# Optimization experiments

Measured on AMD Instinct MI355X. Metric: run time of the kernel, lower is better.

## Reference

```python
import jax, jax.numpy as jnp
import numpy as np

B, L, NC, D = 4, 2048, 4096, 128
ITERS = 4
NHEAD = 8
T = L // 2
C2 = 2 * D


def _ln(x, g, b, eps=1e-5):
    m = jnp.mean(x, axis=-1, keepdims=True)
    v = jnp.var(x, axis=-1, keepdims=True)
    return (x - m) * jax.lax.rsqrt(v + eps) * g + b


def _mlp3(x, W1, b1, W2, b2, W3, b3):
    h = jax.nn.relu(x @ W1 + b1)
    h = jax.nn.relu(h @ W2 + b2)
    return h @ W3 + b3


def _lstm(inp, h, c, Wih, Whh, gi, bi, gh, bh, gc, bc):
    gates = _ln(inp @ Wih, gi, bi) + _ln(h @ Whh, gh, bh)
    i, f, g, o = jnp.split(gates, 4, axis=-1)
    cy = _ln(jax.nn.sigmoid(f) * c + jax.nn.sigmoid(i) * jnp.tanh(g), gc, bc)
    hy = jax.nn.sigmoid(o) * jnp.tanh(cy)
    return hy, cy


def _flip(x):
    # flip matrix with full literal counts == permutation swapping pos/neg halves
    half = x.shape[1] // 2
    return jnp.concatenate([x[:, half:], x[:, :half]], axis=1)


def setup_inputs():
    key = jax.random.key(0)
    ks = iter(jax.random.split(key, 64))
    def xav(fi, fo):
        s = float(np.sqrt(6.0 / (fi + fo)))
        return jax.random.uniform(next(ks), (fi, fo), jnp.float32, -s, s)
    def rn(*shape):
        return jax.random.normal(next(ks), shape, jnp.float32)
    inp = {}
    inp['adjacency_matrices'] = (jax.random.uniform(next(ks), (B, L, NC)) < 0.03).astype(jnp.float32)
    inp['batch_lit_counts'] = jnp.full((B,), L, dtype=jnp.int32)
    inp['L_init'] = rn(1, D) / np.sqrt(D).astype(np.float32)
    inp['C_init'] = rn(1, D) / np.sqrt(D).astype(np.float32)
    for p in ('LC', 'CL'):
        for i in (1, 2, 3):
            inp[p + '_W' + str(i)] = xav(D, D)
            inp[p + '_b' + str(i)] = jnp.full((D,), 0.01, jnp.float32)
    for p, isz in (('Lu', 2 * D), ('Cu', D)):
        inp[p + '_Wih'] = rn(isz, 4 * D)  # torch uses raw randn for LSTM weights
        inp[p + '_Whh'] = rn(D, 4 * D)
        for ln, n in (('lni', 4 * D), ('lnh', 4 * D), ('lnc', D)):
            inp[p + '_' + ln + '_g'] = jnp.ones((n,), jnp.float32)
            inp[p + '_' + ln + '_b'] = jnp.zeros((n,), jnp.float32)
    for p in ('k', 'q', 'v'):
        inp['att_W' + p] = xav(C2, C2)
        inp['att_b' + p] = jnp.zeros((C2,), jnp.float32)
    for p in ('asn', 'vote'):
        inp[p + '_W1'] = xav(C2, D)
        inp[p + '_b1'] = jnp.full((D,), 0.01, jnp.float32)
        inp[p + '_W2'] = xav(D, 1)
        inp[p + '_b2'] = jnp.full((1,), 0.01, jnp.float32)
    return inp


def reference(adjacency_matrices, batch_lit_counts, L_init, C_init,
              LC_W1, LC_b1, LC_W2, LC_b2, LC_W3, LC_b3,
              CL_W1, CL_b1, CL_W2, CL_b2, CL_W3, CL_b3,
              Lu_Wih, Lu_Whh, Lu_lni_g, Lu_lni_b, Lu_lnh_g, Lu_lnh_b, Lu_lnc_g, Lu_lnc_b,
              Cu_Wih, Cu_Whh, Cu_lni_g, Cu_lni_b, Cu_lnh_g, Cu_lnh_b, Cu_lnc_g, Cu_lnc_b,
              att_Wk, att_bk, att_Wq, att_bq, att_Wv, att_bv,
              asn_W1, asn_b1, asn_W2, asn_b2, vote_W1, vote_b1, vote_W2, vote_b2):
    A = adjacency_matrices
    Bb, Ll, Cc = A.shape
    Lh = jnp.broadcast_to(L_init, (Bb, Ll, D))
    Lc = jnp.zeros_like(Lh)
    Ch = jnp.broadcast_to(C_init, (Bb, Cc, D))
    Cxc = jnp.zeros_like(Ch)
    for _ in range(ITERS):
        # literal -> clause messages (gather via A^T)
        LC = jnp.einsum('blc,bld->bcd', A, _mlp3(Lh, LC_W1, LC_b1, LC_W2, LC_b2, LC_W3, LC_b3))
        Ch, Cxc = _lstm(LC, Ch, Cxc, Cu_Wih, Cu_Whh, Cu_lni_g, Cu_lni_b, Cu_lnh_g, Cu_lnh_b, Cu_lnc_g, Cu_lnc_b)
        # clause -> literal messages (scatter via A)
        CL = jnp.einsum('blc,bcd->bld', A, _mlp3(Ch, CL_W1, CL_b1, CL_W2, CL_b2, CL_W3, CL_b3))
        Lh, Lc = _lstm(jnp.concatenate([CL, _flip(Lh)], axis=-1), Lh, Lc,
                       Lu_Wih, Lu_Whh, Lu_lni_g, Lu_lni_b, Lu_lnh_g, Lu_lnh_b, Lu_lnc_g, Lu_lnc_b)
    # readout [h_l ; h_{~l}], positive literals only
    read = jnp.concatenate([Lh, _flip(Lh)], axis=-1)[:, :T]  # [B,T,2D]
    half = batch_lit_counts // 2
    mask = (jnp.arange(T)[None, :] < half[:, None]).astype(read.dtype)  # [B,T]
    read = read * mask[:, :, None]
    hd = C2 // NHEAD
    def heads(x, W, b):
        return (x @ W + b).reshape(Bb, T, NHEAD, hd).transpose(0, 2, 1, 3)
    k = heads(read, att_Wk, att_bk)
    q = heads(read, att_Wq, att_bq)
    v = heads(read, att_Wv, att_bv)
    att = jnp.einsum('bhtd,bhsd->bhts', q, k) * (1.0 / np.sqrt(hd))
    sq = (mask[:, None, :, None] * mask[:, None, None, :]) > 0  # [B,1,T,T]
    att = jnp.where(sq, att, -jnp.inf)
    att = jax.nn.softmax(att, axis=-1)
    att = jnp.where(jnp.isnan(att), 0.0, att)
    y = jnp.einsum('bhts,bhsd->bhtd', att, v).transpose(0, 2, 1, 3).reshape(Bb, T, C2)
    def head_mlp(x, W1, b1, W2, b2):
        return jax.nn.sigmoid(jax.nn.relu(x @ W1 + b1) @ W2 + b2)[..., 0]
    assignments = head_mlp(y, asn_W1, asn_b1, asn_W2, asn_b2) * mask  # [B,T]
    vote_vals = head_mlp(y, vote_W1, vote_b1, vote_W2, vote_b2)
    votes = jnp.sum(vote_vals * mask, axis=1) / jnp.maximum(jnp.sum(mask, axis=1), 1.0)
    return votes, assignments
```

## Files before the change

kernel.cpp:

```cpp
#include <hip/hip_runtime.h>


#define B_    4
#define L_    2048
#define NC_   4096
#define D_    128
#define ITERS_ 4
#define NH_   8
#define T_    1024
#define C2_   256
#define HD_   32
#define BL_   (B_*L_)
#define BNC_  (B_*NC_)

typedef unsigned short u16;
typedef __attribute__((ext_vector_type(8))) short b16x8;
typedef __attribute__((ext_vector_type(4))) float f32x4;

#define MFMA_BF16(a,b,c) __builtin_amdgcn_mfma_f32_16x16x32_bf16((a),(b),(c),0,0,0)

static __device__ __forceinline__ float bf2f(u16 u){
  union{unsigned int i; float f;} x; x.i = ((unsigned int)u) << 16; return x.f;
}
static __device__ __forceinline__ u16 f2bf(float f){
// ... 45 lines not shown
               ksb[NPJ_], dh[NPJ_], dl[NPJ_]; };

__global__ __launch_bounds__(256) void k_prep(PJobs pj, u16* __restrict__ up,
                                              const int* __restrict__ flag){
  int jj = blockIdx.y;
  unsigned n = pj.n[jj];
  unsigned g = blockIdx.x*256 + threadIdx.x;
  if (g >= n) return;
  unsigned j = g & 7, lane = (g>>3)&63;
  unsigned ksb = pj.ksb[jj];
  unsigned ks = (g>>9) & ((1u<<ksb)-1u);
  unsigned nt = g >> (9+ksb);
  unsigned ncol = nt*16 + (lane&15);
  unsigned k = pj.koff[jj] + ks*32 + ((lane>>4)&3)*8 + j;
  unsigned si = k*pj.N[jj] + ncol;
  float v;
  if (*flag) v = bf2f(((const u16*)pj.src[jj])[si]);
  else       v = ((const float*)pj.src[jj])[si];
  u16 h,l; split2(v, h, l);
  up[pj.dh[jj] + g] = h;
  up[pj.dl[jj] + g] = l;
}

__global__ __launch_bounds__(256) void k_init(float* __restrict__ h, float* __restrict__ c,
                                              const float* __restrict__ init, int n){
  int i = blockIdx.x*256 + threadIdx.x;
  if (i < n){ h[i] = init[i & (D_-1)]; c[i] = 0.f; }
}

__global__ void k_zero_u(unsigned* __restrict__ p, int n){
  int i = blockIdx.x*256 + threadIdx.x; if (i < n) p[i] = 0u;
}
__global__ void k_zero(float* p, int n){
  int i = blockIdx.x*64 + threadIdx.x; if (i < n) p[i] = 0.f;
}

__global__ __launch_bounds__(128) void k_pack(const void* __restrict__ A,
    unsigned* __restrict__ bits, unsigned* __restrict__ cnt_l,
    const int* __restrict__ flag){
  const int row = blockIdx.x, w = threadIdx.x;
  unsigned m = 0;
  if (*flag){
    const ushort4* p = (const ushort4*)A + (size_t)row*(NC_/4) + w*8;
    #pragma unroll
    for (int i = 0; i < 8; i++){
      ushort4 u = p[i];
      m |= (unsigned)(u.x != 0) << (i*4);
      m |= (unsigned)(u.y != 0) << (i*4+1);
      m |= (unsigned)(u.z != 0) << (i*4+2);
      m |= (unsigned)(u.w != 0) << (i*4+3);
// ... 62 lines not shown
    int j = __ffs(m) - 1; m &= m - 1;
    val_l[base++] = (u16)(w*32 + j);
    atomicAdd(cnt_c + cb + j, 1u);
  }
}

__global__ __launch_bounds__(256) void k_fill_c(const unsigned* __restrict__ bits,
    const unsigned* __restrict__ off_c, unsigned* __restrict__ cur_c,
    u16* __restrict__ val_c){
  int g = blockIdx.x*256 + threadIdx.x;
  unsigned m = bits[g];
  int row = g >> 7, w = g & 127;
  int b = row >> 11, l = row & (L_-1);
  unsigned cb = ((unsigned)b << 12) + w*32;
  while (m){
    int j = __ffs(m) - 1; m &= m - 1;
    unsigned idx = cb + j;
    unsigned pos = atomicAdd(cur_c + idx, 1u);
    val_c[off_c[idx] + pos] = (u16)l;
  }
}

__global__ __launch_bounds__(256) void k_spmm(const unsigned* __restrict__ off,
    const u16* __restrict__ val, const float* __restrict__ M, float* __restrict__ out,
    int sh1, int sh2){
  int row  = blockIdx.x*4 + (threadIdx.x >> 6);
  int lane = threadIdx.x & 63;
  unsigned p0 = off[row], p1 = off[row+1];
  const float2* Mp = (const float2*)M + (((size_t)(row >> sh1) << sh2) * 64) + lane;
  float x = 0.f, y = 0.f;
  for (unsigned p = p0; p < p1; ++p){
    float2 v = Mp[(size_t)val[p] * 64];
    x += v.x; y += v.y;
  }
  float2 r; r.x = x; r.y = y;
  ((float2*)out)[(size_t)row*64 + lane] = r;
}

__global__ __launch_bounds__(512) void k_mlp3m(const float* __restrict__ X,
    const u16* __restrict__ W1h, const u16* __restrict__ W1l,
    const u16* __restrict__ W2h, const u16* __restrict__ W2l,
    const u16* __restrict__ W3h, const u16* __restrict__ W3l,
    const float* __restrict__ b1, const float* __restrict__ b2,
    const float* __restrict__ b3, float* __restrict__ Y)
{
  __shared__ __align__(16) u16 Ah[32*136];
  __shared__ __align__(16) u16 Al[32*136];
  const int tid = threadIdx.x, lane = tid & 63, wv = tid >> 6;
  const int quad = lane >> 4, l15 = lane & 15;
  const int r0 = blockIdx.x * 32;
  {
    int row = tid >> 4, c0 = (tid & 15)*8;
    const float4* src = (const float4*)(X + (size_t)(r0+row)*128 + c0);
    float4 v0 = src[0], v1 = src[1];
    u16 h,l;
    split2(v0.x,h,l); Ah[row*136+c0]  =h; Al[row*136+c0]  =l;
    split2(v0.y,h,l); Ah[row*136+c0+1]=h; Al[row*136+c0+1]=l;
    split2(v0.z,h,l); Ah[row*136+c0+2]=h; Al[row*136+c0+2]=l;
    split2(v0.w,h,l); Ah[row*136+c0+3]=h; Al[row*136+c0+3]=l;
    split2(v1.x,h,l); Ah[row*136+c0+4]=h; Al[row*136+c0+4]=l;
    split2(v1.y,h,l); Ah[row*136+c0+5]=h; Al[row*136+c0+5]=l;
    split2(v1.z,h,l); Ah[row*136+c0+6]=h; Al[row*136+c0+6]=l;
    split2(v1.w,h,l); Ah[row*136+c0+7]=h; Al[row*136+c0+7]=l;
  }
  __syncthreads();
  const u16* Whs[3] = {W1h, W2h, W3h};
  const u16* Wls[3] = {W1l, W2l, W3l};
  const float* bs[3] = {b1, b2, b3};
  #pragma unroll
  for (int layer = 0; layer < 3; layer++){
    f32x4 acc[2] = {};
    #pragma unroll
    for (int ks = 0; ks < 4; ks++){
      b16x8 a_h[2], a_l[2];
      #pragma unroll
      for (int mt = 0; mt < 2; mt++){
        int ao = (mt*16 + l15)*136 + ks*32 + quad*8;
        a_h[mt] = *(const b16x8*)(Ah + ao);
        a_l[mt] = *(const b16x8*)(Al + ao);
      }
      size_t bo = (size_t)((wv*4 + ks)*64 + lane)*8;
      b16x8 bh = *(const b16x8*)(Whs[layer] + bo);
      b16x8 bl = *(const b16x8*)(Wls[layer] + bo);
      #pragma unroll
      for (int mt = 0; mt < 2; mt++){
        acc[mt] = MFMA_BF16(a_h[mt], bh, acc[mt]);
        acc[mt] = MFMA_BF16(a_h[mt], bl, acc[mt]);
        acc[mt] = MFMA_BF16(a_l[mt], bh, acc[mt]);
      }
    }
    int col = wv*16 + l15;
    if (layer < 2){
      float bb = bs[layer][col];
      __syncthreads();
      #pragma unroll
      for (int mt = 0; mt < 2; mt++)
        #pragma unroll
        for (int r = 0; r < 4; r++){
          int row = mt*16 + quad*4 + r;
          float v = fmaxf(acc[mt][r] + bb, 0.f);
          u16 h,l; split2(v,h,l);
          Ah[row*136 + col] = h; Al[row*136 + col] = l;
        }
      __syncthreads();
    } else {
      float bb = bs[2][col];
      #pragma unroll
      for (int mt = 0; mt < 2; mt++)
        #pragma unroll
        for (int r = 0; r < 4; r++){
          int row = mt*16 + quad*4 + r;
          Y[(size_t)(r0+row)*128 + col] = acc[mt][r] + bb;
        }
    }
  }
}

template<int NSEG>
__global__ __launch_bounds__(512) void k_lstm_mfma(
    const float* __restrict__ A0, const float* __restrict__ A1, const float* __restrict__ A2,
    int flip1,
    const u16* __restrict__ W0h, const u16* __restrict__ W0l,
    const u16* __restrict__ W1h, const u16* __restrict__ W1l,
    const u16* __restrict__ W2h, const u16* __restrict__ W2l,
    const float* __restrict__ lni_g, const float* __restrict__ lni_b,
    const float* __restrict__ lnh_g, const float* __restrict__ lnh_b,
    const float* __restrict__ lnc_g, const float* __restrict__ lnc_b,
    const float* __restrict__ c_in, float* __restrict__ c_out,
    float* __restrict__ h_out)
{
  __shared__ __align__(16) float G[32*516];
  __shared__ float red[8][32][4];
  __shared__ float st[32][4];
  u16* Ah = (u16*)G;
  u16* Al = Ah + 32*136;
  const int tid = threadIdx.x, lane = tid & 63, wv = tid >> 6;
  const int quad = lane >> 4, l15 = lane & 15;
  const int r0 = blockIdx.x * 32;

  f32x4 acc1[2][4] = {}, acc2[2][4] = {};

  #pragma unroll
  for (int s = 0; s < NSEG; ++s){
    const float* Ap = (s==0) ? A0 : ((s==1) ? A1 : A2);
    const u16* Wh = (s==0) ? W0h : ((s==1) ? W1h : W2h);
    const u16* Wl = (s==0) ? W0l : ((s==1) ? W1l : W2l);
    const int fm = (s==1) ? flip1 : 0;
    __syncthreads();
    {
      int row = tid >> 4, c0 = (tid & 15)*8;
      int arow = (r0 + row) ^ fm;
      const float4* src = (const float4*)(Ap + (size_t)arow*128 + c0);
      float4 v0 = src[0], v1 = src[1];
      u16 h,l;
      split2(v0.x,h,l); Ah[row*136+c0]  =h; Al[row*136+c0]  =l;
      split2(v0.y,h,l); Ah[row*136+c0+1]=h; Al[row*136+c0+1]=l;
      split2(v0.z,h,l); Ah[row*136+c0+2]=h; Al[row*136+c0+2]=l;
      split2(v0.w,h,l); Ah[row*136+c0+3]=h; Al[row*136+c0+3]=l;
      split2(v1.x,h,l); Ah[row*136+c0+4]=h; Al[row*136+c0+4]=l;
      split2(v1.y,h,l); Ah[row*136+c0+5]=h; Al[row*136+c0+5]=l;
      split2(v1.z,h,l); Ah[row*136+c0+6]=h; Al[row*136+c0+6]=l;
      split2(v1.w,h,l); Ah[row*136+c0+7]=h; Al[row*136+c0+7]=l;
    }
    __syncthreads();
    f32x4 (*accp)[4] = (s == NSEG-1) ? acc2 : acc1;
    #pragma unroll
    for (int ks = 0; ks < 4; ks++){
      b16x8 a_h[2], a_l[2];
      #pragma unroll
      for (int mt = 0; mt < 2; mt++){
        int ao = (mt*16 + l15)*136 + ks*32 + quad*8;
        a_h[mt] = *(const b16x8*)(Ah + ao);
        a_l[mt] = *(const b16x8*)(Al + ao);
      }
      #pragma unroll
      for (int ntl = 0; ntl < 4; ntl++){
        int nt = wv*4 + ntl;
        size_t bo = (size_t)((nt*4 + ks)*64 + lane)*8;
        b16x8 bh = *(const b16x8*)(Wh + bo);
        b16x8 bl = *(const b16x8*)(Wl + bo);
        #pragma unroll
        for (int mt = 0; mt < 2; mt++){
          accp[mt][ntl] = MFMA_BF16(a_h[mt], bh, accp[mt][ntl]);
          accp[mt][ntl] = MFMA_BF16(a_h[mt], bl, accp[mt][ntl]);
          accp[mt][ntl] = MFMA_BF16(a_l[mt], bh, accp[mt][ntl]);
        }
      }
    }
  }

  #pragma unroll
  for (int mt = 0; mt < 2; mt++)
    #pragma unroll
    for (int r = 0; r < 4; r++){
      float s1=0.f, q1=0.f, s2=0.f, q2=0.f;
      #pragma unroll
// ... 51 lines not shown
  #pragma unroll
  for (int i = 0; i < 4; i++){
    int row = wv*4 + i;
    int rg = r0 + row;
    float cp[2], sc = 0.f, qc = 0.f;
    #pragma unroll
    for (int jj = 0; jj < 2; jj++){
      int c = lane + 64*jj;
      float iv = sigm(G[row*516 + c]);
      float fv = sigm(G[row*516 + 128 + c]);
      float gv = tanhf(G[row*516 + 256 + c]);
      cp[jj] = fv * c_in[(size_t)rg*128 + c] + iv*gv;
      sc += cp[jj]; qc += cp[jj]*cp[jj];
    }
    #pragma unroll
    for (int m = 1; m < 64; m <<= 1){ sc += __shfl_xor(sc, m); qc += __shfl_xor(qc, m); }
    float mc = sc*i128, vc = fmaxf(qc*i128 - mc*mc, 0.f), rsc = rsqrtf(vc + 1e-5f);
    #pragma unroll
    for (int jj = 0; jj < 2; jj++){
      int c = lane + 64*jj;
      float cy = (cp[jj]-mc)*rsc*(jj ? lcg1 : lcg0) + (jj ? lcb1 : lcb0);
      c_out[(size_t)rg*128 + c] = cy;
      float ov = sigm(G[row*516 + 384 + c]);
      h_out[(size_t)rg*128 + c] = ov*tanhf(cy);
    }
  }
}

template<int NT, int NSPLIT, int KK32, int ACT, int GATHER>
__global__ __launch_bounds__(512) void k_gemm_mfma(const float* __restrict__ A,
    const u16* __restrict__ Wh, const u16* __restrict__ Wl,
    const float* __restrict__ bias, float* __restrict__ Y,
    const int* __restrict__ counts)
{
  const int NTOT = NSPLIT*8*NT*16;
  const int LDA = KK32*32 + 8;
  __shared__ __align__(16) u16 Ah[32*(KK32*32+8)];
  __shared__ __align__(16) u16 Al[32*(KK32*32+8)];
  const int tid = threadIdx.x, lane = tid & 63, wv = tid >> 6;
  const int quad = lane >> 4, l15 = lane & 15;
  const int r0 = blockIdx.x * 32, by = blockIdx.y;
  {
    int row = tid >> 4, c0 = (tid & 15)*(KK32*2);
    if (GATHER){
      int r = r0 + row; int b = r >> 10; int t = r & 1023;
      int half = counts[b] / 2; if (half > T_) half = T_;
      float msk = (t < half) ? 1.f : 0.f;
      #pragma unroll
      for (int q4 = 0; q4 < KK32/2; q4++){
        int c = c0 + q4*4;
        const float* src = A + ((size_t)(b*L_ + t + ((c >= 128) ? T_ : 0))*128 + (c & 127));
        float4 v = *(const float4*)src;
        u16 h,l;
        split2(v.x*msk,h,l); Ah[row*LDA+c]  =h; Al[row*LDA+c]  =l;
        split2(v.y*msk,h,l); Ah[row*LDA+c+1]=h; Al[row*LDA+c+1]=l;
        split2(v.z*msk,h,l); Ah[row*LDA+c+2]=h; Al[row*LDA+c+2]=l;
        split2(v.w*msk,h,l); Ah[row*LDA+c+3]=h; Al[row*LDA+c+3]=l;
      }
    } else {
      const float4* src = (const float4*)(A + (size_t)(r0+row)*(KK32*32) + c0);
      #pragma unroll
      for (int q4 = 0; q4 < KK32/2; q4++){
        float4 v = src[q4]; int c = c0 + q4*4;
        u16 h,l;
        split2(v.x,h,l); Ah[row*LDA+c]  =h; Al[row*LDA+c]  =l;
        split2(v.y,h,l); Ah[row*LDA+c+1]=h; Al[row*LDA+c+1]=l;
        split2(v.z,h,l); Ah[row*LDA+c+2]=h; Al[row*LDA+c+2]=l;
        split2(v.w,h,l); Ah[row*LDA+c+3]=h; Al[row*LDA+c+3]=l;
      }
    }
  }
  __syncthreads();
  f32x4 acc[2][NT] = {};
  #pragma unroll
  for (int ks = 0; ks < KK32; ks++){
    b16x8 a_h[2], a_l[2];
    #pragma unroll
    for (int mt = 0; mt < 2; mt++){
      int ao = (mt*16 + l15)*LDA + ks*32 + quad*8;
      a_h[mt] = *(const b16x8*)(Ah + ao);
      a_l[mt] = *(const b16x8*)(Al + ao);
    }
    #pragma unroll
    for (int ntl = 0; ntl < NT; ntl++){
      int nt = by*(8*NT) + wv*NT + ntl;
      size_t bo = (size_t)((nt*KK32 + ks)*64 + lane)*8;
      b16x8 bh = *(const b16x8*)(Wh + bo);
      b16x8 bl = *(const b16x8*)(Wl + bo);
      #pragma unroll
      for (int mt = 0; mt < 2; mt++){
        acc[mt][ntl] = MFMA_BF16(a_h[mt], bh, acc[mt][ntl]);
        acc[mt][ntl] = MFMA_BF16(a_h[mt], bl, acc[mt][ntl]);
        acc[mt][ntl] = MFMA_BF16(a_l[mt], bh, acc[mt][ntl]);
      }
    }
  }
  #pragma unroll
  for (int mt = 0; mt < 2; mt++)
    #pragma unroll
    for (int ntl = 0; ntl < NT; ntl++){
      int colg = by*(8*NT*16) + wv*(NT*16) + ntl*16 + l15;
      float bb = bias[colg];
      #pragma unroll
      for (int r = 0; r < 4; r++){
        int row = mt*16 + quad*4 + r;
        float v = acc[mt][ntl][r] + bb;
        if (ACT) v = fmaxf(v, 0.f);
        Y[(size_t)(r0+row)*NTOT + colg] = v;
      }
    }
}

__global__ __launch_bounds__(512) void k_qkv_gemm(const float* __restrict__ A,
    const u16* __restrict__ Wh, const u16* __restrict__ Wl,
    const float* __restrict__ bias,
    u16* __restrict__ Qh, u16* __restrict__ Ql,
    u16* __restrict__ Kh, u16* __restrict__ Kl,
    u16* __restrict__ Vth, u16* __restrict__ Vtl,
    const int* __restrict__ counts)
{
  const int KK32 = 8, NT = 3;
  const int LDA = KK32*32 + 8;
  __shared__ __align__(16) u16 Ah[32*(KK32*32+8)];
  __shared__ __align__(16) u16 Al[32*(KK32*32+8)];
  const int tid = threadIdx.x, lane = tid & 63, wv = tid >> 6;
  const int quad = lane >> 4, l15 = lane & 15;
  const int r0 = blockIdx.x * 32, by = blockIdx.y;
  {
    int row = tid >> 4, c0 = (tid & 15)*(KK32*2);
    int r = r0 + row; int b = r >> 10; int t = r & 1023;
    int half = counts[b] / 2; if (half > T_) half = T_;
    float msk = (t < half) ? 1.f : 0.f;
    #pragma unroll
    for (int q4 = 0; q4 < KK32/2; q4++){
      int c = c0 + q4*4;
      const float* src = A + ((size_t)(b*L_ + t + ((c >= 128) ? T_ : 0))*128 + (c & 127));
      float4 v = *(const float4*)src;
      u16 h,l;
      split2(v.x*msk,h,l); Ah[row*LDA+c]  =h; Al[row*LDA+c]  =l;
      split2(v.y*msk,h,l); Ah[row*LDA+c+1]=h; Al[row*LDA+c+1]=l;
      split2(v.z*msk,h,l); Ah[row*LDA+c+2]=h; Al[row*LDA+c+2]=l;
      split2(v.w*msk,h,l); Ah[row*LDA+c+3]=h; Al[row*LDA+c+3]=l;
    }
  }
  __syncthreads();
  f32x4 acc[2][NT] = {};
  #pragma unroll
  for (int ks = 0; ks < KK32; ks++){
    b16x8 a_h[2], a_l[2];
    #pragma unroll
    for (int mt = 0; mt < 2; mt++){
      int ao = (mt*16 + l15)*LDA + ks*32 + quad*8;
      a_h[mt] = *(const b16x8*)(Ah + ao);
      a_l[mt] = *(const b16x8*)(Al + ao);
    }
    #pragma unroll
    for (int ntl = 0; ntl < NT; ntl++){
      int nt = by*(8*NT) + wv*NT + ntl;
      size_t bo = (size_t)((nt*KK32 + ks)*64 + lane)*8;
      b16x8 bh = *(const b16x8*)(Wh + bo);
      b16x8 bl = *(const b16x8*)(Wl + bo);
      #pragma unroll
      for (int mt = 0; mt < 2; mt++){
        acc[mt][ntl] = MFMA_BF16(a_h[mt], bh, acc[mt][ntl]);
        acc[mt][ntl] = MFMA_BF16(a_h[mt], bl, acc[mt][ntl]);
        acc[mt][ntl] = MFMA_BF16(a_l[mt], bh, acc[mt][ntl]);
      }
    }
  }
  #pragma unroll
  for (int mt = 0; mt < 2; mt++)
    #pragma unroll
    for (int ntl = 0; ntl < NT; ntl++){
      int colg = by*(8*NT*16) + wv*(NT*16) + ntl*16 + l15;
      float bb = bias[colg];
      #pragma unroll
      for (int r = 0; r < 4; r++){
        int row = r0 + mt*16 + quad*4 + r;
        int bI = row >> 10, t = row & 1023;
        float v = acc[mt][ntl][r] + bb;
        u16 hh, ll; split2(v, hh, ll);
        if (colg < 256){
          int h8 = colg >> 5, k = colg & 31;
          size_t idx = ((size_t)(bI*NH_ + h8)*1024 + t)*32 + k;
          Qh[idx] = hh; Ql[idx] = ll;
        } else if (colg < 512){
          int c = colg - 256; int h8 = c >> 5, k = c & 31;
          size_t idx = ((size_t)(bI*NH_ + h8)*1024 + t)*32 + k;
          Kh[idx] = hh; Kl[idx] = ll;
        } else {
          int c = colg - 512; int h8 = c >> 5, n = c & 31;
          size_t idx = ((size_t)(bI*NH_ + h8)*32 + n)*1024 + t;
          Vth[idx] = hh; Vtl[idx] = ll;
        }
      }
    }
}

__global__ __launch_bounds__(256) void k_attn_mfma(
    const u16* __restrict__ Qh, const u16* __restrict__ Ql,
    const u16* __restrict__ Kh, const u16* __restrict__ Kl,
    const u16* __restrict__ Vth, const u16* __restrict__ Vtl,
    const int* __restrict__ counts, float* __restrict__ y)
{
  const int b = blockIdx.z, h = blockIdx.y, t0 = blockIdx.x*64;
  int half = counts[b] / 2; if (half > T_) half = T_; if (half < 0) half = 0;
  const int tid = threadIdx.x, lane = tid & 63, w = tid >> 6;
  const int quad = lane >> 4, l15 = lane & 15;
  __shared__ __align__(16) u16 Pb[4][2][16*72];
  const int tw = t0 + w*16;
  const size_t bh = (size_t)(b*NH_ + h)*32768;
  const u16* qhb = Qh + bh; const u16* qlb = Ql + bh;
  const u16* khb = Kh + bh; const u16* klb = Kl + bh;
  const u16* vhb = Vth + bh; const u16* vlb = Vtl + bh;

  b16x8 qah = *(const b16x8*)(qhb + (size_t)(tw + l15)*32 + quad*8);
  b16x8 qal = *(const b16x8*)(qlb + (size_t)(tw + l15)*32 + quad*8);

  f32x4 accO[2] = {};
  float mst[4], lst[4];
  #pragma unroll
  for (int r = 0; r < 4; r++){ mst[r] = -3e38f; lst[r] = 0.f; }
  const float scale = 0.17677669529663687f;
  const int ntile = (t0 < half) ? ((half + 63) >> 6) : 0;

  for (int st = 0; st < ntile; ++st){
// ... 46 lines not shown
      accO[1][r] *= alpha[r];
    }
    #pragma unroll
    for (int kc = 0; kc < 2; kc++){
      b16x8 ph = *(const b16x8*)&Pb[w][0][l15*72 + kc*32 + quad*8];
      b16x8 pl = *(const b16x8*)&Pb[w][1][l15*72 + kc*32 + quad*8];
      #pragma unroll
      for (int nt = 0; nt < 2; nt++){
        const size_t vo = (size_t)(nt*16 + l15)*1024 + s0 + kc*32 + quad*8;
        b16x8 vh8 = *(const b16x8*)(vhb + vo);
        b16x8 vl8 = *(const b16x8*)(vlb + vo);
        accO[nt] = MFMA_BF16(ph, vh8, accO[nt]);
        accO[nt] = MFMA_BF16(ph, vl8, accO[nt]);
        accO[nt] = MFMA_BF16(pl, vh8, accO[nt]);
      }
    }
  }

  #pragma unroll
  for (int r = 0; r < 4; r++){
    int t = tw + quad*4 + r;
    float inv = (t < half && lst[r] > 0.f) ? 1.f/lst[r] : 0.f;
    #pragma unroll
    for (int nt = 0; nt < 2; nt++)
      y[(size_t)(b*T_ + t)*C2_ + h*HD_ + nt*16 + l15] = accO[nt][r]*inv;
  }
}

__global__ __launch_bounds__(128) void k_final(const float* __restrict__ hv,
    const float* __restrict__ aW2, const float* __restrict__ ab2,
    const float* __restrict__ vW2, const float* __restrict__ vb2,
    const int* __restrict__ counts, void* __restrict__ outv,
    float* __restrict__ vote_sum, const int* __restrict__ flag)
{
  int row = blockIdx.x, tid = threadIdx.x;
  int b = row / T_, t = row - b*T_;
  int half = counts[b] / 2; if (half > T_) half = T_;
  float pa = hv[(size_t)row*256 + tid]       * aW2[tid];
  float pv = hv[(size_t)row*256 + 128 + tid] * vW2[tid];
  #pragma unroll
  for (int off = 32; off > 0; off >>= 1){ pa += __shfl_down(pa, off); pv += __shfl_down(pv, off); }
  __shared__ float r[2][2];
  int wid = tid >> 6, lane = tid & 63;
  if (lane == 0){ r[0][wid] = pa; r[1][wid] = pv; }
  __syncthreads();
  if (tid == 0){
    float a  = sigm(r[0][0] + r[0][1] + ab2[0]);
    float vv = sigm(r[1][0] + r[1][1] + vb2[0]);
    bool mk = (t < half);
// ... 25 lines not shown

  const size_t M1 = (size_t)1048576;
  const size_t NEED = (5*M1 + M1 + 2*M1 + 2*M1 + 700416 + 16416 + 8224
                       + 16384 + 8192 + 520000 + 520000 + 32) * sizeof(float);
  if (ws_size < NEED) return;

  float* ws = (float*)d_ws;
  float* R    = ws;
  float* Lc   = R + 5*M1;
  float* Ch   = Lc + M1;
  float* Cc   = Ch + 2*M1;
  float* wp   = Cc + 2*M1;
  unsigned* off_c = (unsigned*)(wp + 700416);
  unsigned* off_l = off_c + 16416;
  unsigned* cnt_c = off_l + 8224;
  unsigned* cnt_l = cnt_c + 16384;
  u16* val_c = (u16*)(cnt_l + 8192);
  u16* val_l = (u16*)((float*)val_c + 520000);
  float* tail = (float*)val_l + 520000;
  float* vote_sum = tail;
  int* flag = (int*)(tail + 8);
  unsigned* bits = (unsigned*)R;

  float* R0 = R, *R1 = R + M1, *R2 = R + 2*M1, *R3 = R + 3*M1, *R4 = R + 4*M1;

  k_detect<<<1, 256, 0, stream>>>((const unsigned int*)A_adj, flag);

  CJobs cj;
  int ncj = 0;
  unsigned off = 0;
  auto cadd = [&](int idx, unsigned n)->float*{
    cj.src[ncj] = d_in[idx]; cj.n[ncj] = n; cj.off[ncj] = off;
    float* p = wp + off; off += (n + 3u) & ~3u; ncj++; return p;
  };
  float* Linit = cadd(2, 128);
  float* Cinit = cadd(3, 128);
  float *LC_b1 = cadd(5, 128), *LC_b2 = cadd(7, 128), *LC_b3 = cadd(9, 128);
  float *CL_b1 = cadd(11,128), *CL_b2 = cadd(13,128), *CL_b3 = cadd(15,128);
  float *Lu_lni_g = cadd(18,512), *Lu_lni_b = cadd(19,512);
  float *Lu_lnh_g = cadd(20,512), *Lu_lnh_b = cadd(21,512);
  float *Lu_lnc_g = cadd(22,128), *Lu_lnc_b = cadd(23,128);
  float *Cu_lni_g = cadd(26,512), *Cu_lni_b = cadd(27,512);
  float *Cu_lnh_g = cadd(28,512), *Cu_lnh_b = cadd(29,512);
  float *Cu_lnc_g = cadd(30,128), *Cu_lnc_b = cadd(31,128);
  float *asn_W2 = cadd(40,128), *asn_b2 = cadd(41,1);
  float *vote_W2 = cadd(44,128), *vote_b2 = cadd(45,1);
  float* bqkv = wp + off;
// ... 32 lines not shown
  solo(16,65536,512,0,  2,&lwa_h,&lwa_l);
  solo(16,65536,512,128,2,&lwb_h,&lwb_l);
  solo(17,65536,512,0,2,&lwhh_h,&lwhh_l);
  const u16* wqkv_h = up + uoff;
  const u16* wqkv_l = up + uoff + 196608;
  padd(34, 65536, 256, 0, 3, uoff,           uoff+196608);
  padd(32, 65536, 256, 0, 3, uoff+65536,     uoff+196608+65536);
  padd(36, 65536, 256, 0, 3, uoff+131072,    uoff+196608+131072);
  uoff += 393216;
  const u16* whv_h = up + uoff;
  const u16* whv_l = up + uoff + 65536;
  padd(38, 32768, 128, 0, 3, uoff,        uoff+65536);
  padd(42, 32768, 128, 0, 3, uoff+32768,  uoff+65536+32768);
  uoff += 131072;
  { dim3 g(256, NPJ_); k_prep<<<g, 256, 0, stream>>>(pj, up, flag); }

  k_zero_u<<<(16384+255)/256, 256, 0, stream>>>(cnt_c, 16384);
  k_pack<<<BL_, 128, 0, stream>>>(A_adj, bits, cnt_l, flag);
  k_scan<<<1, 256, 0, stream>>>(cnt_l, off_l, 8192);
  k_fill_l<<<BL_, 128, 0, stream>>>(bits, off_l, val_l, cnt_c);
  k_scan<<<1, 256, 0, stream>>>(cnt_c, off_c, 16384);
  k_fill_c<<<4096, 256, 0, stream>>>(bits, off_c, cnt_c, val_c);

  k_init<<<(BL_*D_)/256, 256, 0, stream>>>(R0, Lc, Linit, BL_*D_);
  k_init<<<(BNC_*D_)/256, 256, 0, stream>>>(Ch, Cc, Cinit, BNC_*D_);

  for (int it = 0; it < ITERS_; ++it){
    bool ev = ((it & 1) == 0);
    float* cur  = ev ? R0 : R4;
    float* msgL = ev ? R1 : R0;
    float* LCb  = ev ? R2 : R1;
    float* msgC = LCb;
    float* CLb  = ev ? R1 : R3;
    float* nxt  = ev ? R4 : R0;

    k_mlp3m<<<BL_/32, 512, 0, stream>>>(cur, lc1h,lc1l, lc2h,lc2l, lc3h,lc3l,
                                        LC_b1, LC_b2, LC_b3, msgL);
    k_spmm<<<BNC_/4, 256, 0, stream>>>(off_c, val_c, msgL, LCb, 12, 11);
    k_lstm_mfma<2><<<BNC_/32, 512, 0, stream>>>(LCb, Ch, nullptr, 0,
        cwih_h, cwih_l, cwhh_h, cwhh_l, nullptr, nullptr,
        Cu_lni_g, Cu_lni_b, Cu_lnh_g, Cu_lnh_b, Cu_lnc_g, Cu_lnc_b, Cc, Cc, Ch);
    k_mlp3m<<<BNC_/32, 512, 0, stream>>>(Ch, cl1h,cl1l, cl2h,cl2l, cl3h,cl3l,
                                         CL_b1, CL_b2, CL_b3, msgC);
    k_spmm<<<BL_/4, 256, 0, stream>>>(off_l, val_l, msgC, CLb, 11, 12);
    k_lstm_mfma<3><<<BL_/32, 512, 0, stream>>>(CLb, cur, cur, 1024,
        lwa_h, lwa_l, lwb_h, lwb_l, lwhh_h, lwhh_l,
        Lu_lni_g, Lu_lni_b, Lu_lnh_g, Lu_lnh_b, Lu_lnc_g, Lu_lnc_b, Lc, Lc, nxt);
  }
  float* Lh = R0;

  u16* qk = (u16*)Ch;
  u16* Qh_ = qk;           u16* Ql_ = qk + 1048576;
  u16* Kh_ = qk + 2097152; u16* Kl_ = qk + 3145728;
  u16* vt = (u16*)Cc;
  u16* Vth_ = vt;          u16* Vtl_ = vt + 1048576;
  float* yb = R1;
  float* hv = R2;

  { dim3 g((B_*T_)/32, 2);
    k_qkv_gemm<<<g, 512, 0, stream>>>(Lh, wqkv_h, wqkv_l, bqkv,
                                      Qh_, Ql_, Kh_, Kl_, Vth_, Vtl_, counts); }
  { dim3 g(T_/64, NH_, B_);
    k_attn_mfma<<<g, 256, 0, stream>>>(Qh_, Ql_, Kh_, Kl_, Vth_, Vtl_, counts, yb); }
  { dim3 g((B_*T_)/32, 2);
    k_gemm_mfma<1,2,8,1,0><<<g, 512, 0, stream>>>(yb, whv_h, whv_l, bhv, hv, counts); }
  k_zero<<<1, 64, 0, stream>>>(vote_sum, B_);
  k_final<<<B_*T_, 128, 0, stream>>>(hv, asn_W2, asn_b2, vote_W2, vote_b2,
                                     counts, d_out, vote_sum, flag);
  k_votes<<<1, 64, 0, stream>>>(vote_sum, counts, d_out, flag);
}
```

Before: 1.593 ms.

## Store activations pre-split as bf16 hi/lo pairs to skip LDS staging

```diff
diff --git a/kernel.cpp b/kernel.cpp
--- a/kernel.cpp
+++ b/kernel.cpp
@@ -91,10 +91,13 @@
   up[pj.dl[jj] + g] = l;
 }
 
-__global__ __launch_bounds__(256) void k_init(float* __restrict__ h, float* __restrict__ c,
-                                              const float* __restrict__ init, int n){
+__global__ __launch_bounds__(256) void k_init_h(u16* __restrict__ hh, u16* __restrict__ hl,
+    float* __restrict__ c, const float* __restrict__ init, int n){
   int i = blockIdx.x*256 + threadIdx.x;
-  if (i < n){ h[i] = init[i & (D_-1)]; c[i] = 0.f; }
+  if (i < n){
+    u16 h,l; split2(init[i & (D_-1)], h, l);
+    hh[i] = h; hl[i] = l; c[i] = 0.f;
+  }
 }
 
 __global__ void k_zero_u(unsigned* __restrict__ p, int n){
@@ -203,8 +206,8 @@
 }
 
 __global__ __launch_bounds__(256) void k_spmm(const unsigned* __restrict__ off,
-    const u16* __restrict__ val, const float* __restrict__ M, float* __restrict__ out,
-    int sh1, int sh2){
+    const u16* __restrict__ val, const float* __restrict__ M,
+    u16* __restrict__ outh, u16* __restrict__ outl, int sh1, int sh2){
   int row  = blockIdx.x*4 + (threadIdx.x >> 6);
   int lane = threadIdx.x & 63;
   unsigned p0 = off[row], p1 = off[row+1];
@@ -214,11 +217,13 @@
     float2 v = Mp[(size_t)val[p] * 64];
     x += v.x; y += v.y;
   }
-  float2 r; r.x = x; r.y = y;
-  ((float2*)out)[(size_t)row*64 + lane] = r;
-}
-
-__global__ __launch_bounds__(512) void k_mlp3m(const float* __restrict__ X,
+  u16 hx,lx,hy,ly; split2(x,hx,lx); split2(y,hy,ly);
+  ((unsigned*)outh)[(size_t)row*64 + lane] = (unsigned)hx | ((unsigned)hy << 16);
+  ((unsigned*)outl)[(size_t)row*64 + lane] = (unsigned)lx | ((unsigned)ly << 16);
+}
+
+__global__ __launch_bounds__(512) void k_mlp3m(const u16* __restrict__ Xh,
+    const u16* __restrict__ Xl,
     const u16* __restrict__ W1h, const u16* __restrict__ W1l,
     const u16* __restrict__ W2h, const u16* __restrict__ W2l,
     const u16* __restrict__ W3h, const u16* __restrict__ W3l,
@@ -230,21 +235,6 @@
   const int tid = threadIdx.x, lane = tid & 63, wv = tid >> 6;
   const int quad = lane >> 4, l15 = lane & 15;
   const int r0 = blockIdx.x * 32;
-  {
-    int row = tid >> 4, c0 = (tid & 15)*8;
-    const float4* src = (const float4*)(X + (size_t)(r0+row)*128 + c0);
-    float4 v0 = src[0], v1 = src[1];
-    u16 h,l;
-    split2(v0.x,h,l); Ah[row*136+c0]  =h; Al[row*136+c0]  =l;
-    split2(v0.y,h,l); Ah[row*136+c0+1]=h; Al[row*136+c0+1]=l;
-    split2(v0.z,h,l); Ah[row*136+c0+2]=h; Al[row*136+c0+2]=l;
-    split2(v0.w,h,l); Ah[row*136+c0+3]=h; Al[row*136+c0+3]=l;
-    split2(v1.x,h,l); Ah[row*136+c0+4]=h; Al[row*136+c0+4]=l;
-    split2(v1.y,h,l); Ah[row*136+c0+5]=h; Al[row*136+c0+5]=l;
-    split2(v1.z,h,l); Ah[row*136+c0+6]=h; Al[row*136+c0+6]=l;
-    split2(v1.w,h,l); Ah[row*136+c0+7]=h; Al[row*136+c0+7]=l;
-  }
-  __syncthreads();
   const u16* Whs[3] = {W1h, W2h, W3h};
   const u16* Wls[3] = {W1l, W2l, W3l};
   const float* bs[3] = {b1, b2, b3};
@@ -256,9 +246,15 @@
       b16x8 a_h[2], a_l[2];
       #pragma unroll
       for (int mt = 0; mt < 2; mt++){
-        int ao = (mt*16 + l15)*136 + ks*32 + quad*8;
-        a_h[mt] = *(const b16x8*)(Ah + ao);
-        a_l[mt] = *(const b16x8*)(Al + ao);
+        if (layer == 0){
+          size_t ao = (size_t)(r0 + mt*16 + l15)*128 + ks*32 + quad*8;
+          a_h[mt] = *(const b16x8*)(Xh + ao);
+          a_l[mt] = *(const b16x8*)(Xl + ao);
+        } else {
+          int ao = (mt*16 + l15)*136 + ks*32 + quad*8;
+          a_h[mt] = *(const b16x8*)(Ah + ao);
+          a_l[mt] = *(const b16x8*)(Al + ao);
+        }
       }
       size_t bo = (size_t)((wv*4 + ks)*64 + lane)*8;
       b16x8 bh = *(const b16x8*)(Whs[layer] + bo);
@@ -299,7 +295,9 @@
 
 template<int NSEG>
 __global__ __launch_bounds__(512) void k_lstm_mfma(
-    const float* __restrict__ A0, const float* __restrict__ A1, const float* __restrict__ A2,
+    const u16* __restrict__ A0h, const u16* __restrict__ A0l,
+    const u16* __restrict__ A1h, const u16* __restrict__ A1l,
+    const u16* __restrict__ A2h, const u16* __restrict__ A2l,
     int flip1,
     const u16* __restrict__ W0h, const u16* __restrict__ W0l,
     const u16* __restrict__ W1h, const u16* __restrict__ W1l,
@@ -308,13 +306,11 @@
     const float* __restrict__ lnh_g, const float* __restrict__ lnh_b,
     const float* __restrict__ lnc_g, const float* __restrict__ lnc_b,
     const float* __restrict__ c_in, float* __restrict__ c_out,
-    float* __restrict__ h_out)
+    u16* __restrict__ h_outh, u16* __restrict__ h_outl)
 {
   __shared__ __align__(16) float G[32*516];
   __shared__ float red[8][32][4];
   __shared__ float st[32][4];
-  u16* Ah = (u16*)G;
-  u16* Al = Ah + 32*136;
   const int tid = threadIdx.x, lane = tid & 63, wv = tid >> 6;
   const int quad = lane >> 4, l15 = lane & 15;
   const int r0 = blockIdx.x * 32;
@@ -323,36 +319,20 @@
 
   #pragma unroll
   for (int s = 0; s < NSEG; ++s){
-    const float* Ap = (s==0) ? A0 : ((s==1) ? A1 : A2);
-    const u16* Wh = (s==0) ? W0h : ((s==1) ? W1h : W2h);
-    const u16* Wl = (s==0) ? W0l : ((s==1) ? W1l : W2l);
+    const u16* Aph = (s==0) ? A0h : ((s==1) ? A1h : A2h);
+    const u16* Apl = (s==0) ? A0l : ((s==1) ? A1l : A2l);
+    const u16* Wh  = (s==0) ? W0h : ((s==1) ? W1h : W2h);
+    const u16* Wl  = (s==0) ? W0l : ((s==1) ? W1l : W2l);
     const int fm = (s==1) ? flip1 : 0;
-    __syncthreads();
-    {
-      int row = tid >> 4, c0 = (tid & 15)*8;
-      int arow = (r0 + row) ^ fm;
-      const float4* src = (const float4*)(Ap + (size_t)arow*128 + c0);
-      float4 v0 = src[0], v1 = src[1];
-      u16 h,l;
-      split2(v0.x,h,l); Ah[row*136+c0]  =h; Al[row*136+c0]  =l;
-      split2(v0.y,h,l); Ah[row*136+c0+1]=h; Al[row*136+c0+1]=l;
-      split2(v0.z,h,l); Ah[row*136+c0+2]=h; Al[row*136+c0+2]=l;
-      split2(v0.w,h,l); Ah[row*136+c0+3]=h; Al[row*136+c0+3]=l;
-      split2(v1.x,h,l); Ah[row*136+c0+4]=h; Al[row*136+c0+4]=l;
-      split2(v1.y,h,l); Ah[row*136+c0+5]=h; Al[row*136+c0+5]=l;
-      split2(v1.z,h,l); Ah[row*136+c0+6]=h; Al[row*136+c0+6]=l;
-      split2(v1.w,h,l); Ah[row*136+c0+7]=h; Al[row*136+c0+7]=l;
-    }
-    __syncthreads();
     f32x4 (*accp)[4] = (s == NSEG-1) ? acc2 : acc1;
     #pragma unroll
     for (int ks = 0; ks < 4; ks++){
       b16x8 a_h[2], a_l[2];
       #pragma unroll
       for (int mt = 0; mt < 2; mt++){
-        int ao = (mt*16 + l15)*136 + ks*32 + quad*8;
-        a_h[mt] = *(const b16x8*)(Ah + ao);
-        a_l[mt] = *(const b16x8*)(Al + ao);
+        size_t ao = (size_t)((r0 + mt*16 + l15) ^ fm)*128 + ks*32 + quad*8;
+        a_h[mt] = *(const b16x8*)(Aph + ao);
+        a_l[mt] = *(const b16x8*)(Apl + ao);
       }
       #pragma unroll
       for (int ntl = 0; ntl < 4; ntl++){
@@ -450,96 +430,16 @@
       float cy = (cp[jj]-mc)*rsc*(jj ? lcg1 : lcg0) + (jj ? lcb1 : lcb0);
       c_out[(size_t)rg*128 + c] = cy;
       float ov = sigm(G[row*516 + 384 + c]);
-      h_out[(size_t)rg*128 + c] = ov*tanhf(cy);
-    }
-  }
-}
-
-template<int NT, int NSPLIT, int KK32, int ACT, int GATHER>
-__global__ __launch_bounds__(512) void k_gemm_mfma(const float* __restrict__ A,
-    const u16* __restrict__ Wh, const u16* __restrict__ Wl,
-    const float* __restrict__ bias, float* __restrict__ Y,
-    const int* __restrict__ counts)
-{
-  const int NTOT = NSPLIT*8*NT*16;
-  const int LDA = KK32*32 + 8;
-  __shared__ __align__(16) u16 Ah[32*(KK32*32+8)];
-  __shared__ __align__(16) u16 Al[32*(KK32*32+8)];
-  const int tid = threadIdx.x, lane = tid & 63, wv = tid >> 6;
-  const int quad = lane >> 4, l15 = lane & 15;
-  const int r0 = blockIdx.x * 32, by = blockIdx.y;
-  {
-    int row = tid >> 4, c0 = (tid & 15)*(KK32*2);
-    if (GATHER){
-      int r = r0 + row; int b = r >> 10; int t = r & 1023;
-      int half = counts[b] / 2; if (half > T_) half = T_;
-      float msk = (t < half) ? 1.f : 0.f;
-      #pragma unroll
-      for (int q4 = 0; q4 < KK32/2; q4++){
-        int c = c0 + q4*4;
-        const float* src = A + ((size_t)(b*L_ + t + ((c >= 128) ? T_ : 0))*128 + (c & 127));
-        float4 v = *(const float4*)src;
-        u16 h,l;
-        split2(v.x*msk,h,l); Ah[row*LDA+c]  =h; Al[row*LDA+c]  =l;
-        split2(v.y*msk,h,l); Ah[row*LDA+c+1]=h; Al[row*LDA+c+1]=l;
-        split2(v.z*msk,h,l); Ah[row*LDA+c+2]=h; Al[row*LDA+c+2]=l;
-        split2(v.w*msk,h,l); Ah[row*LDA+c+3]=h; Al[row*LDA+c+3]=l;
-      }
-    } else {
-      const float4* src = (const float4*)(A + (size_t)(r0+row)*(KK32*32) + c0);
-      #pragma unroll
-      for (int q4 = 0; q4 < KK32/2; q4++){
-        float4 v = src[q4]; int c = c0 + q4*4;
-        u16 h,l;
-        split2(v.x,h,l); Ah[row*LDA+c]  =h; Al[row*LDA+c]  =l;
-        split2(v.y,h,l); Ah[row*LDA+c+1]=h; Al[row*LDA+c+1]=l;
-        split2(v.z,h,l); Ah[row*LDA+c+2]=h; Al[row*LDA+c+2]=l;
-        split2(v.w,h,l); Ah[row*LDA+c+3]=h; Al[row*LDA+c+3]=l;
-      }
-    }
-  }
-  __syncthreads();
-  f32x4 acc[2][NT] = {};
-  #pragma unroll
-  for (int ks = 0; ks < KK32; ks++){
-    b16x8 a_h[2], a_l[2];
-    #pragma unroll
-    for (int mt = 0; mt < 2; mt++){
-      int ao = (mt*16 + l15)*LDA + ks*32 + quad*8;
-      a_h[mt] = *(const b16x8*)(Ah + ao);
-      a_l[mt] = *(const b16x8*)(Al + ao);
-    }
-    #pragma unroll
-    for (int ntl = 0; ntl < NT; ntl++){
-      int nt = by*(8*NT) + wv*NT + ntl;
-      size_t bo = (size_t)((nt*KK32 + ks)*64 + lane)*8;
-      b16x8 bh = *(const b16x8*)(Wh + bo);
-      b16x8 bl = *(const b16x8*)(Wl + bo);
-      #pragma unroll
-      for (int mt = 0; mt < 2; mt++){
-        acc[mt][ntl] = MFMA_BF16(a_h[mt], bh, acc[mt][ntl]);
-        acc[mt][ntl] = MFMA_BF16(a_h[mt], bl, acc[mt][ntl]);
-        acc[mt][ntl] = MFMA_BF16(a_l[mt], bh, acc[mt][ntl]);
-      }
-    }
-  }
-  #pragma unroll
-  for (int mt = 0; mt < 2; mt++)
-    #pragma unroll
-    for (int ntl = 0; ntl < NT; ntl++){
-      int colg = by*(8*NT*16) + wv*(NT*16) + ntl*16 + l15;
-      float bb = bias[colg];
-      #pragma unroll
-      for (int r = 0; r < 4; r++){
-        int row = mt*16 + quad*4 + r;
-        float v = acc[mt][ntl][r] + bb;
-        if (ACT) v = fmaxf(v, 0.f);
-        Y[(size_t)(r0+row)*NTOT + colg] = v;
-      }
-    }
-}
-
-__global__ __launch_bounds__(512) void k_qkv_gemm(const float* __restrict__ A,
+      float hval = ov*tanhf(cy);
+      u16 hh, ll; split2(hval, hh, ll);
+      h_outh[(size_t)rg*128 + c] = hh;
+      h_outl[(size_t)rg*128 + c] = ll;
+    }
+  }
+}
+
+__global__ __launch_bounds__(512) void k_qkv_gemm(const u16* __restrict__ Lhh,
+    const u16* __restrict__ Lhl,
     const u16* __restrict__ Wh, const u16* __restrict__ Wl,
     const float* __restrict__ bias,
     u16* __restrict__ Qh, u16* __restrict__ Ql,
@@ -547,45 +447,37 @@
     u16* __restrict__ Vth, u16* __restrict__ Vtl,
     const int* __restrict__ counts)
 {
-  const int KK32 = 8, NT = 3;
-  const int LDA = KK32*32 + 8;
-  __shared__ __align__(16) u16 Ah[32*(KK32*32+8)];
-  __shared__ __align__(16) u16 Al[32*(KK32*32+8)];
+  const int NT = 3;
   const int tid = threadIdx.x, lane = tid & 63, wv = tid >> 6;
   const int quad = lane >> 4, l15 = lane & 15;
   const int r0 = blockIdx.x * 32, by = blockIdx.y;
-  {
-    int row = tid >> 4, c0 = (tid & 15)*(KK32*2);
-    int r = r0 + row; int b = r >> 10; int t = r & 1023;
+  size_t off0[2], off1[2];
+  bool mk[2];
+  #pragma unroll
+  for (int mt = 0; mt < 2; mt++){
+    int r = r0 + mt*16 + l15;
+    int b = r >> 10, t = r & 1023;
     int half = counts[b] / 2; if (half > T_) half = T_;
-    float msk = (t < half) ? 1.f : 0.f;
-    #pragma unroll
-    for (int q4 = 0; q4 < KK32/2; q4++){
-      int c = c0 + q4*4;
-      const float* src = A + ((size_t)(b*L_ + t + ((c >= 128) ? T_ : 0))*128 + (c & 127));
-      float4 v = *(const float4*)src;
-      u16 h,l;
-      split2(v.x*msk,h,l); Ah[row*LDA+c]  =h; Al[row*LDA+c]  =l;
-      split2(v.y*msk,h,l); Ah[row*LDA+c+1]=h; Al[row*LDA+c+1]=l;
-      split2(v.z*msk,h,l); Ah[row*LDA+c+2]=h; Al[row*LDA+c+2]=l;
-      split2(v.w*msk,h,l); Ah[row*LDA+c+3]=h; Al[row*LDA+c+3]=l;
-    }
-  }
-  __syncthreads();
+    mk[mt] = (t < half);
+    off0[mt] = (size_t)(b*L_ + t)*128;
+    off1[mt] = (size_t)(b*L_ + t + T_)*128;
+  }
+  const b16x8 z = {};
   f32x4 acc[2][NT] = {};
   #pragma unroll
-  for (int ks = 0; ks < KK32; ks++){
+  for (int ks = 0; ks < 8; ks++){
+    const int kk = (ks & 3)*32 + quad*8;
     b16x8 a_h[2], a_l[2];
     #pragma unroll
     for (int mt = 0; mt < 2; mt++){
-      int ao = (mt*16 + l15)*LDA + ks*32 + quad*8;
-      a_h[mt] = *(const b16x8*)(Ah + ao);
-      a_l[mt] = *(const b16x8*)(Al + ao);
+      size_t ao = ((ks < 4) ? off0[mt] : off1[mt]) + kk;
+      a_h[mt] = mk[mt] ? *(const b16x8*)(Lhh + ao) : z;
+      a_l[mt] = mk[mt] ? *(const b16x8*)(Lhl + ao) : z;
     }
     #pragma unroll
     for (int ntl = 0; ntl < NT; ntl++){
       int nt = by*(8*NT) + wv*NT + ntl;
-      size_t bo = (size_t)((nt*KK32 + ks)*64 + lane)*8;
+      size_t bo = (size_t)((nt*8 + ks)*64 + lane)*8;
       b16x8 bh = *(const b16x8*)(Wh + bo);
       b16x8 bl = *(const b16x8*)(Wl + bo);
       #pragma unroll
@@ -629,7 +521,8 @@
     const u16* __restrict__ Qh, const u16* __restrict__ Ql,
     const u16* __restrict__ Kh, const u16* __restrict__ Kl,
     const u16* __restrict__ Vth, const u16* __restrict__ Vtl,
-    const int* __restrict__ counts, float* __restrict__ y)
+    const int* __restrict__ counts,
+    u16* __restrict__ yh, u16* __restrict__ yl)
 {
   const int b = blockIdx.z, h = blockIdx.y, t0 = blockIdx.x*64;
   int half = counts[b] / 2; if (half > T_) half = T_; if (half < 0) half = 0;
@@ -722,9 +615,52 @@
     int t = tw + quad*4 + r;
     float inv = (t < half && lst[r] > 0.f) ? 1.f/lst[r] : 0.f;
     #pragma unroll
-    for (int nt = 0; nt < 2; nt++)
-      y[(size_t)(b*T_ + t)*C2_ + h*HD_ + nt*16 + l15] = accO[nt][r]*inv;
-  }
+    for (int nt = 0; nt < 2; nt++){
+      u16 hh, ll; split2(accO[nt][r]*inv, hh, ll);
+      size_t yi = (size_t)(b*T_ + t)*C2_ + h*HD_ + nt*16 + l15;
+      yh[yi] = hh; yl[yi] = ll;
+    }
+  }
+}
+
+__global__ __launch_bounds__(512) void k_hv_gemm(const u16* __restrict__ yh,
+    const u16* __restrict__ yl,
+    const u16* __restrict__ Wh, const u16* __restrict__ Wl,
+    const float* __restrict__ bias, float* __restrict__ Y)
+{
+  const int tid = threadIdx.x, lane = tid & 63, wv = tid >> 6;
+  const int quad = lane >> 4, l15 = lane & 15;
+  const int r0 = blockIdx.x * 32, by = blockIdx.y;
+  f32x4 acc[2] = {};
+  #pragma unroll
+  for (int ks = 0; ks < 8; ks++){
+    b16x8 a_h[2], a_l[2];
+    #pragma unroll
+    for (int mt = 0; mt < 2; mt++){
+      size_t ao = (size_t)(r0 + mt*16 + l15)*256 + ks*32 + quad*8;
+      a_h[mt] = *(const b16x8*)(yh + ao);
+      a_l[mt] = *(const b16x8*)(yl + ao);
+    }
+    int nt = by*8 + wv;
+    size_t bo = (size_t)((nt*8 + ks)*64 + lane)*8;
+    b16x8 bh = *(const b16x8*)(Wh + bo);
+    b16x8 bl = *(const b16x8*)(Wl + bo);
+    #pragma unroll
+    for (int mt = 0; mt < 2; mt++){
+      acc[mt] = MFMA_BF16(a_h[mt], bh, acc[mt]);
+      acc[mt] = MFMA_BF16(a_h[mt], bl, acc[mt]);
+      acc[mt] = MFMA_BF16(a_l[mt], bh, acc[mt]);
+    }
+  }
+  int colg = by*128 + wv*16 + l15;
+  float bb = bias[colg];
+  #pragma unroll
+  for (int mt = 0; mt < 2; mt++)
+    #pragma unroll
+    for (int r = 0; r < 4; r++){
+      int row = mt*16 + quad*4 + r;
+      Y[(size_t)(r0+row)*256 + colg] = fmaxf(acc[mt][r] + bb, 0.f);
+    }
 }
 
 __global__ __launch_bounds__(128) void k_final(const float* __restrict__ hv,
@@ -796,7 +732,11 @@
   int* flag = (int*)(tail + 8);
   unsigned* bits = (unsigned*)R;
 
-  float* R0 = R, *R1 = R + M1, *R2 = R + 2*M1, *R3 = R + 3*M1, *R4 = R + 4*M1;
+  auto SH = [&](int i)->u16*{ return (u16*)(R + i*M1); };
+  auto SL = [&](int i)->u16*{ return (u16*)(R + i*M1) + M1; };
+
+  u16* Chh = (u16*)Ch; u16* Chl = Chh + 2*M1;
+  float* R0 = R, *R1 = R + M1, *R2 = R + 2*M1;
 
   k_detect<<<1, 256, 0, stream>>>((const unsigned int*)A_adj, flag);
 
@@ -875,48 +815,49 @@
   k_scan<<<1, 256, 0, stream>>>(cnt_c, off_c, 16384);
   k_fill_c<<<4096, 256, 0, stream>>>(bits, off_c, cnt_c, val_c);
 
-  k_init<<<(BL_*D_)/256, 256, 0, stream>>>(R0, Lc, Linit, BL_*D_);
-  k_init<<<(BNC_*D_)/256, 256, 0, stream>>>(Ch, Cc, Cinit, BNC_*D_);
+  k_init_h<<<(BL_*D_)/256, 256, 0, stream>>>(SH(0), SL(0), Lc, Linit, BL_*D_);
+  k_init_h<<<(BNC_*D_)/256, 256, 0, stream>>>(Chh, Chl, Cc, Cinit, BNC_*D_);
 
   for (int it = 0; it < ITERS_; ++it){
     bool ev = ((it & 1) == 0);
-    float* cur  = ev ? R0 : R4;
+    u16 *curh = ev ? SH(0) : SH(4), *curl = ev ? SL(0) : SL(4);
     float* msgL = ev ? R1 : R0;
-    float* LCb  = ev ? R2 : R1;
-    float* msgC = LCb;
-    float* CLb  = ev ? R1 : R3;
-    float* nxt  = ev ? R4 : R0;
-
-    k_mlp3m<<<BL_/32, 512, 0, stream>>>(cur, lc1h,lc1l, lc2h,lc2l, lc3h,lc3l,
+    u16 *LCbh = ev ? (u16*)(R+2*M1) : (u16*)(R+1*M1);
+    u16 *LCbl = ev ? (u16*)(R+3*M1) : (u16*)(R+2*M1);
+    float* msgC = ev ? (R+2*M1) : (R+1*M1);
+    u16 *CLbh = ev ? SH(1) : SH(3), *CLbl = ev ? SL(1) : SL(3);
+    u16 *nxth = ev ? SH(4) : SH(0), *nxtl = ev ? SL(4) : SL(0);
+
+    k_mlp3m<<<BL_/32, 512, 0, stream>>>(curh, curl, lc1h,lc1l, lc2h,lc2l, lc3h,lc3l,
                                         LC_b1, LC_b2, LC_b3, msgL);
-    k_spmm<<<BNC_/4, 256, 0, stream>>>(off_c, val_c, msgL, LCb, 12, 11);
-    k_lstm_mfma<2><<<BNC_/32, 512, 0, stream>>>(LCb, Ch, nullptr, 0,
+    k_spmm<<<BNC_/4, 256, 0, stream>>>(off_c, val_c, msgL, LCbh, LCbl, 12, 11);
+    k_lstm_mfma<2><<<BNC_/32, 512, 0, stream>>>(LCbh, LCbl, Chh, Chl, nullptr, nullptr, 0,
         cwih_h, cwih_l, cwhh_h, cwhh_l, nullptr, nullptr,
-        Cu_lni_g, Cu_lni_b, Cu_lnh_g, Cu_lnh_b, Cu_lnc_g, Cu_lnc_b, Cc, Cc, Ch);
-    k_mlp3m<<<BNC_/32, 512, 0, stream>>>(Ch, cl1h,cl1l, cl2h,cl2l, cl3h,cl3l,
+        Cu_lni_g, Cu_lni_b, Cu_lnh_g, Cu_lnh_b, Cu_lnc_g, Cu_lnc_b, Cc, Cc, Chh, Chl);
+    k_mlp3m<<<BNC_/32, 512, 0, stream>>>(Chh, Chl, cl1h,cl1l, cl2h,cl2l, cl3h,cl3l,
                                          CL_b1, CL_b2, CL_b3, msgC);
-    k_spmm<<<BL_/4, 256, 0, stream>>>(off_l, val_l, msgC, CLb, 11, 12);
-    k_lstm_mfma<3><<<BL_/32, 512, 0, stream>>>(CLb, cur, cur, 1024,
+    k_spmm<<<BL_/4, 256, 0, stream>>>(off_l, val_l, msgC, CLbh, CLbl, 11, 12);
+    k_lstm_mfma<3><<<BL_/32, 512, 0, stream>>>(CLbh, CLbl, curh, curl, curh, curl, 1024,
         lwa_h, lwa_l, lwb_h, lwb_l, lwhh_h, lwhh_l,
-        Lu_lni_g, Lu_lni_b, Lu_lnh_g, Lu_lnh_b, Lu_lnc_g, Lu_lnc_b, Lc, Lc, nxt);
-  }
-  float* Lh = R0;
+        Lu_lni_g, Lu_lni_b, Lu_lnh_g, Lu_lnh_b, Lu_lnc_g, Lu_lnc_b, Lc, Lc, nxth, nxtl);
+  }
+  u16* Lhh = SH(0);  u16* Lhl = SL(0);
 
   u16* qk = (u16*)Ch;
   u16* Qh_ = qk;           u16* Ql_ = qk + 1048576;
   u16* Kh_ = qk + 2097152; u16* Kl_ = qk + 3145728;
   u16* vt = (u16*)Cc;
   u16* Vth_ = vt;          u16* Vtl_ = vt + 1048576;
-  float* yb = R1;
+  u16* yh_ = (u16*)R1;     u16* yl_ = (u16*)R1 + 1048576;
   float* hv = R2;
 
   { dim3 g((B_*T_)/32, 2);
-    k_qkv_gemm<<<g, 512, 0, stream>>>(Lh, wqkv_h, wqkv_l, bqkv,
+    k_qkv_gemm<<<g, 512, 0, stream>>>(Lhh, Lhl, wqkv_h, wqkv_l, bqkv,
                                       Qh_, Ql_, Kh_, Kl_, Vth_, Vtl_, counts); }
   { dim3 g(T_/64, NH_, B_);
-    k_attn_mfma<<<g, 256, 0, stream>>>(Qh_, Ql_, Kh_, Kl_, Vth_, Vtl_, counts, yb); }
+    k_attn_mfma<<<g, 256, 0, stream>>>(Qh_, Ql_, Kh_, Kl_, Vth_, Vtl_, counts, yh_, yl_); }
   { dim3 g((B_*T_)/32, 2);
-    k_gemm_mfma<1,2,8,1,0><<<g, 512, 0, stream>>>(yb, whv_h, whv_l, bhv, hv, counts); }
+    k_hv_gemm<<<g, 512, 0, stream>>>(yh_, yl_, whv_h, whv_l, bhv, hv); }
   k_zero<<<1, 64, 0, stream>>>(vote_sum, B_);
   k_final<<<B_*T_, 128, 0, stream>>>(hv, asn_W2, asn_b2, vote_W2, vote_b2,
                                      counts, d_out, vote_sum, flag);
```

Measured after the change: 1.678 ms. 5.4% more time.
